# Performance work log

Measured on AMD Instinct MI355X. Metric: run time of the kernel, lower is better.

## Reference

```python
import jax, jax.numpy as jnp
import numpy as np

LN_EPS = 1e-5


def setup_inputs() -> dict:
    key = jax.random.key(0)
    k1, k2, k3, k4, k5 = jax.random.split(key, 5)
    N, E, D = 50000, 800000, 128
    feature = jax.random.normal(k1, (N, D), dtype=jnp.float32)
    snorm_n = jax.random.uniform(k2, (N, 1), dtype=jnp.float32)
    W = jax.random.normal(k3, (D, D), dtype=jnp.float32) * (1.0 / np.sqrt(D))
    ln_scale = jnp.ones((D,), dtype=jnp.float32)
    ln_bias = jnp.zeros((D,), dtype=jnp.float32)
    src = jax.random.randint(k4, (E,), 0, N, dtype=jnp.int64)
    dst = jax.random.randint(k5, (E,), 0, N, dtype=jnp.int64)
    return {"feature": feature, "snorm_n": snorm_n, "W": W,
            "ln_scale": ln_scale, "ln_bias": ln_bias, "src": src, "dst": dst}


def reference(feature, snorm_n, W, ln_scale, ln_bias, src, dst):
    N = feature.shape[0]
    # copy_src message + sum reduce: gather src features, segment-sum into dst
    msgs = feature[src]                                   # [E, D]
    h = jax.ops.segment_sum(msgs, dst, num_segments=N)    # [N, D]
    # NodeApplyModule: Linear(in_dim, out_dim, bias=False)
    h = h @ W.T                                           # [N, D]
    # graph norm
    h = h * snorm_n
    # layer norm over feature dim
    mu = jnp.mean(h, axis=-1, keepdims=True)
    var = jnp.mean(jnp.square(h - mu), axis=-1, keepdims=True)
    h = (h - mu) * jax.lax.rsqrt(var + LN_EPS) * ln_scale + ln_bias
    # activation (relu); dropout p=0 is identity in eval
    h = jax.nn.relu(h)
    return h
```

## Files before the change

kernel.cpp:

```cpp
#include <hip/hip_runtime.h>

typedef __attribute__((ext_vector_type(8))) short bf16x8;
typedef __attribute__((ext_vector_type(4))) short short4v;
typedef __attribute__((ext_vector_type(4))) float f32x4;

__device__ inline short f2bf(float x) {
    unsigned u = __builtin_bit_cast(unsigned, x);
    u += 0x7fffu + ((u >> 16) & 1u);
    return (short)(u >> 16);
}
__device__ inline float bflo(unsigned v) { return __builtin_bit_cast(float, v << 16); }
__device__ inline float bfhi(unsigned v) { return __builtin_bit_cast(float, v & 0xffff0000u); }

#define LDW  136
#define CAP  64
#define NBINS_MAX 196
#define BINSHIFT 8
#define CAPB 4864
#define RING 32
#define RSTR 33

#define POISON 0xAAAAAAAAu
__device__ inline unsigned decode_cur(unsigned raw) {
    unsigned d = raw - POISON;
    if (d < 65536u) return d;
    if (raw < 65536u) return raw;
    return 0;
}

__global__ __launch_bounds__(256) void k1_gemm_bin(
        const float* __restrict__ feat, const float* __restrict__ W,
        unsigned short* __restrict__ ft, int ntiles, int nGemm,
        const int* __restrict__ src, const int* __restrict__ dst,
        unsigned* __restrict__ binCur,
        unsigned* __restrict__ binsG,
        int E, int nbins) {
    __shared__ __align__(16) char smem[34816];
    int tid = threadIdx.x;

    if ((int)blockIdx.x < nGemm) {
        short* Wlds = (short*)smem;
        const float4* W4 = (const float4*)W;
        for (int i = tid; i < 128 * 32; i += 256) {
            int r = i >> 5, c4 = (i & 31) << 2;
            float4 w = W4[i];
            short4v s = { f2bf(w.x), f2bf(w.y), f2bf(w.z), f2bf(w.w) };
            *(short4v*)&Wlds[r * LDW + c4] = s;
        }
        __syncthreads();

        int wave = tid >> 6, lane = tid & 63;
        int l15 = lane & 15, quad = lane >> 4;

        for (int tile = blockIdx.x * 4 + wave; tile < ntiles; tile += nGemm * 4) {
            int row0 = tile << 4;
            f32x4 acc[8];
            #pragma unroll
            for (int c = 0; c < 8; ++c) acc[c] = (f32x4){0.f, 0.f, 0.f, 0.f};

            const float* arow = feat + (long long)(row0 + l15) * 128;
            #pragma unroll
            for (int t = 0; t < 4; ++t) {
                const float4* ap = (const float4*)(arow + t * 32 + quad * 8);
                float4 a0 = ap[0], a1 = ap[1];
                bf16x8 af = { f2bf(a0.x), f2bf(a0.y), f2bf(a0.z), f2bf(a0.w),
                              f2bf(a1.x), f2bf(a1.y), f2bf(a1.z), f2bf(a1.w) };
                const short* wp = &Wlds[l15 * LDW + t * 32 + quad * 8];
                #pragma unroll
                for (int c = 0; c < 8; ++c) {
                    bf16x8 bf = *(const bf16x8*)(wp + c * 16 * LDW);
                    acc[c] = __builtin_amdgcn_mfma_f32_16x16x32_bf16(af, bf, acc[c], 0, 0, 0);
                }
            }
            #pragma unroll
            for (int c = 0; c < 8; ++c) {
                int col = (c << 4) + l15;
                #pragma unroll
                for (int j = 0; j < 4; ++j)
                    ft[(long long)(row0 + quad * 4 + j) * 128 + col] =
                        (unsigned short)f2bf(acc[c][j]);
            }
        }
    } else {
        unsigned* stage = (unsigned*)smem;
        int* bcnt = (int*)(smem + NBINS_MAX * RSTR * 4);
        int* bflu = bcnt + NBINS_MAX;
        for (int i = tid; i < nbins; i += 256) { bcnt[i] = 0; bflu[i] = 0; }
        __syncthreads();

        int bid  = blockIdx.x - nGemm;
        int nB   = gridDim.x - nGemm;
        int step = nB * 256;
        int iters = (E - bid * 256 + step - 1) / step;

        int e = bid * 256 + tid;
        int d = (e < E) ? dst[e] : -1;
        int s = (e < E) ? src[e] : 0;

        for (int it = 0; it < iters; ++it) {
            int en = e + step;
            bool more = (it + 1 < iters) && (en < E);
            int dn = more ? dst[en] : -1;
            int sn = more ? src[en] : 0;

            if (d >= 0) {
                int bin = d >> BINSHIFT;
                unsigned pack = ((unsigned)(d & 255) << 16) | (unsigned)s;
                int pos = atomicAdd(&bcnt[bin], 1);
                stage[bin * RSTR + (pos & (RING - 1))] = pack;
            }
            __syncthreads();
            for (int b = tid; b < nbins; b += 256) {
                int c = bcnt[b], f = bflu[b];
                if (c - f >= 16) {
                    unsigned g = decode_cur(atomicAdd(&binCur[b], 16u));
                    if (g + 16 <= CAPB) {
                        unsigned* dp = binsG + (size_t)b * CAPB + g;
                        int s0 = f & (RING - 1);
                        #pragma unroll
                        for (int k = 0; k < 16; ++k)
                            dp[k] = stage[b * RSTR + s0 + k];
                    }
                    bflu[b] = f + 16;
                }
            }
            __syncthreads();
            e = en; d = dn; s = sn;
        }
        for (int b = tid; b < nbins; b += 256) {
            int c = bcnt[b], f = bflu[b];
            int rem = c - f;
            if (rem > 0) {
                unsigned g = decode_cur(atomicAdd(&binCur[b], (unsigned)rem));
                for (int k = 0; k < rem; ++k)
                    if (g + k < CAPB)
                        binsG[(size_t)b * CAPB + g + k] =
                            stage[b * RSTR + ((f + k) & (RING - 1))];
            }
        }
    }
}

__global__ __launch_bounds__(256) void k2_gather_ln(
        const unsigned short* __restrict__ ft,
        const unsigned* __restrict__ binCur, const unsigned* __restrict__ binsG,
        const float* __restrict__ snorm, const float* __restrict__ ln_scale,
        const float* __restrict__ ln_bias, float2* __restrict__ out,
        int N) {
    __shared__ unsigned short buck[32 * CAP];
    __shared__ int bcnt[32];
    int tid = threadIdx.x;
    int bin = blockIdx.x >> 3, oct = blockIdx.x & 7;
    int nlo = (bin << BINSHIFT) + (oct << 5);

    if (tid < 32) bcnt[tid] = 0;
    __syncthreads();

    int cnt_b = (int)decode_cur(binCur[bin]);
    if (cnt_b > CAPB) cnt_b = CAPB;
    const unsigned* bp = binsG + (size_t)bin * CAPB;
    for (int i = tid; i < cnt_b; i += 256) {
        unsigned pack = bp[i];
        int dl = pack >> 16;
        if ((dl >> 5) == oct) {
            int local = dl & 31;
            int slot = atomicAdd(&bcnt[local], 1);
            if (slot < CAP) buck[local * CAP + slot] = (unsigned short)(pack & 0xffffu);
        }
    }
    __syncthreads();

    int wave = tid >> 6, lane = tid & 63;
    const unsigned* ftp = (const unsigned*)ft;
    float2 g = ((const float2*)ln_scale)[lane];
    float2 b = ((const float2*)ln_bias)[lane];

    for (int k = 0; k < 8; ++k) {
        int local = wave * 8 + k;
        int node = nlo + local;
        if (node >= N) break;
        int deg = bcnt[local];
        if (deg > CAP) deg = CAP;
        const unsigned short* lst = &buck[local * CAP];

        float ax = 0.f, ay = 0.f;
        int i = 0;
        for (; i + 8 <= deg; i += 8) {
            ushort4 a4 = *(const ushort4*)&lst[i];
            ushort4 b4 = *(const ushort4*)&lst[i + 4];
            unsigned v0 = ftp[(int)a4.x * 64 + lane];
            unsigned v1 = ftp[(int)a4.y * 64 + lane];
            unsigned v2 = ftp[(int)a4.z * 64 + lane];
            unsigned v3 = ftp[(int)a4.w * 64 + lane];
            unsigned v4 = ftp[(int)b4.x * 64 + lane];
            unsigned v5 = ftp[(int)b4.y * 64 + lane];
            unsigned v6 = ftp[(int)b4.z * 64 + lane];
            unsigned v7 = ftp[(int)b4.w * 64 + lane];
            ax += bflo(v0) + bflo(v1) + bflo(v2) + bflo(v3)
                + bflo(v4) + bflo(v5) + bflo(v6) + bflo(v7);
            ay += bfhi(v0) + bfhi(v1) + bfhi(v2) + bfhi(v3)
                + bfhi(v4) + bfhi(v5) + bfhi(v6) + bfhi(v7);
        }
        for (; i + 4 <= deg; i += 4) {
            ushort4 s4 = *(const ushort4*)&lst[i];
            unsigned v0 = ftp[(int)s4.x * 64 + lane];
            unsigned v1 = ftp[(int)s4.y * 64 + lane];
            unsigned v2 = ftp[(int)s4.z * 64 + lane];
            unsigned v3 = ftp[(int)s4.w * 64 + lane];
            ax += bflo(v0) + bflo(v1) + bflo(v2) + bflo(v3);
            ay += bfhi(v0) + bfhi(v1) + bfhi(v2) + bfhi(v3);
        }
        for (; i < deg; ++i) {
            unsigned v = ftp[(int)lst[i] * 64 + lane];
            ax += bflo(v); ay += bfhi(v);
        }

        float sn = snorm[node];
        float vx = ax * sn, vy = ay * sn;
        float s1 = vx + vy, s2 = vx * vx + vy * vy;
        #pragma unroll
        for (int m = 1; m < 64; m <<= 1) {
            s1 += __shfl_xor(s1, m, 64);
            s2 += __shfl_xor(s2, m, 64);
        }
        float mu = s1 * (1.0f / 128.0f);
        float var = s2 * (1.0f / 128.0f) - mu * mu;
        float rs = rsqrtf(var + 1e-5f);
        float ox = fmaxf((vx - mu) * rs * g.x + b.x, 0.f);
        float oy = fmaxf((vy - mu) * rs * g.y + b.y, 0.f);
        out[(long long)node * 64 + lane] = make_float2(ox, oy);
    }
}

#define POISON_CNT_BOUND 4096u
__device__ inline int decode_cnt(unsigned raw) {
    unsigned d = raw - POISON;
    if (d < POISON_CNT_BOUND) return (int)d;
    if (raw < POISON_CNT_BOUND) return (int)raw;
    return 0;
}

__global__ __launch_bounds__(256) void fused_gemm_bucket(
        const float* __restrict__ feat, const float* __restrict__ W,
        unsigned short* __restrict__ ft, int ntiles, int nGemm,
        const int* __restrict__ src, const int* __restrict__ dst,
        int* __restrict__ cnt, unsigned short* __restrict__ esrc, int E) {
    __shared__ short Wlds[128 * LDW];
    int tid = threadIdx.x;
    if ((int)blockIdx.x < nGemm) {
        const float4* W4 = (const float4*)W;
        for (int i = tid; i < 128 * 32; i += 256) {
            int r = i >> 5, c4 = (i & 31) << 2;
            float4 w = W4[i];
            short4v s = { f2bf(w.x), f2bf(w.y), f2bf(w.z), f2bf(w.w) };
            *(short4v*)&Wlds[r * LDW + c4] = s;
        }
        __syncthreads();
        int wave = tid >> 6, lane = tid & 63;
        int l15 = lane & 15, quad = lane >> 4;
        for (int tile = blockIdx.x * 4 + wave; tile < ntiles; tile += nGemm * 4) {
            int row0 = tile << 4;
            f32x4 acc[8];
            #pragma unroll
            for (int c = 0; c < 8; ++c) acc[c] = (f32x4){0.f, 0.f, 0.f, 0.f};
            const float* arow = feat + (long long)(row0 + l15) * 128;
            #pragma unroll
            for (int t = 0; t < 4; ++t) {
                const float4* ap = (const float4*)(arow + t * 32 + quad * 8);
                float4 a0 = ap[0], a1 = ap[1];
                bf16x8 af = { f2bf(a0.x), f2bf(a0.y), f2bf(a0.z), f2bf(a0.w),
                              f2bf(a1.x), f2bf(a1.y), f2bf(a1.z), f2bf(a1.w) };
                const short* wp = &Wlds[l15 * LDW + t * 32 + quad * 8];
                #pragma unroll
                for (int c = 0; c < 8; ++c) {
                    bf16x8 bf = *(const bf16x8*)(wp + c * 16 * LDW);
                    acc[c] = __builtin_amdgcn_mfma_f32_16x16x32_bf16(af, bf, acc[c], 0, 0, 0);
                }
            }
            #pragma unroll
            for (int c = 0; c < 8; ++c) {
                int col = (c << 4) + l15;
                #pragma unroll
                for (int j = 0; j < 4; ++j)
                    ft[(long long)(row0 + quad * 4 + j) * 128 + col] =
                        (unsigned short)f2bf(acc[c][j]);
            }
        }
    } else {
        int bid = blockIdx.x - nGemm;
        int nBucket = gridDim.x - nGemm;
        for (int e = bid * 256 + tid; e < E; e += nBucket * 256) {
            int d = dst[e];
            int s = src[e];
            unsigned raw = (unsigned)atomicAdd(&cnt[d], 1);
            int slot = decode_cnt(raw);
            if (slot < CAP) esrc[d * CAP + slot] = (unsigned short)s;
        }
    }
}

__global__ __launch_bounds__(256) void gather_ln(
        const unsigned short* __restrict__ ft, const int* __restrict__ cnt,
        const unsigned short* __restrict__ esrc,
        const float* __restrict__ snorm, const float* __restrict__ ln_scale,
        const float* __restrict__ ln_bias, float2* __restrict__ out, int N) {
    int node = blockIdx.x * 4 + (threadIdx.x >> 6);
    if (node >= N) return;
    int lane = threadIdx.x & 63;
    int deg = decode_cnt((unsigned)cnt[node]);
    if (deg > CAP) deg = CAP;
    const unsigned short* lst = esrc + node * CAP;
    const unsigned* ftp = (const unsigned*)ft;
    float ax = 0.f, ay = 0.f;
    int i = 0;
    for (; i + 8 <= deg; i += 8) {
        ushort4 a4 = *(const ushort4*)&lst[i];
        ushort4 b4 = *(const ushort4*)&lst[i + 4];
        unsigned v0 = ftp[(int)a4.x * 64 + lane];
        unsigned v1 = ftp[(int)a4.y * 64 + lane];
        unsigned v2 = ftp[(int)a4.z * 64 + lane];
        unsigned v3 = ftp[(int)a4.w * 64 + lane];
        unsigned v4 = ftp[(int)b4.x * 64 + lane];
        unsigned v5 = ftp[(int)b4.y * 64 + lane];
        unsigned v6 = ftp[(int)b4.z * 64 + lane];
        unsigned v7 = ftp[(int)b4.w * 64 + lane];
        ax += bflo(v0) + bflo(v1) + bflo(v2) + bflo(v3)
            + bflo(v4) + bflo(v5) + bflo(v6) + bflo(v7);
        ay += bfhi(v0) + bfhi(v1) + bfhi(v2) + bfhi(v3)
            + bfhi(v4) + bfhi(v5) + bfhi(v6) + bfhi(v7);
    }
    for (; i + 4 <= deg; i += 4) {
        ushort4 s4 = *(const ushort4*)&lst[i];
        unsigned v0 = ftp[(int)s4.x * 64 + lane];
        unsigned v1 = ftp[(int)s4.y * 64 + lane];
        unsigned v2 = ftp[(int)s4.z * 64 + lane];
        unsigned v3 = ftp[(int)s4.w * 64 + lane];
        ax += bflo(v0) + bflo(v1) + bflo(v2) + bflo(v3);
        ay += bfhi(v0) + bfhi(v1) + bfhi(v2) + bfhi(v3);
    }
    for (; i < deg; ++i) {
        unsigned v = ftp[(int)lst[i] * 64 + lane];
        ax += bflo(v); ay += bfhi(v);
    }
    float sn = snorm[node];
    float vx = ax * sn, vy = ay * sn;
    float s1 = vx + vy, s2 = vx * vx + vy * vy;
    #pragma unroll
    for (int m = 1; m < 64; m <<= 1) {
        s1 += __shfl_xor(s1, m, 64);
        s2 += __shfl_xor(s2, m, 64);
    }
    float mu = s1 * (1.0f / 128.0f);
    float var = s2 * (1.0f / 128.0f) - mu * mu;
    float rs = rsqrtf(var + 1e-5f);
    float2 g = ((const float2*)ln_scale)[lane];
    float2 b = ((const float2*)ln_bias)[lane];
    float ox = fmaxf((vx - mu) * rs * g.x + b.x, 0.f);
    float oy = fmaxf((vy - mu) * rs * g.y + b.y, 0.f);
    out[(long long)node * 64 + lane] = make_float2(ox, oy);
}

__global__ __launch_bounds__(256) void scatter_add_kernel(
        const float4* __restrict__ feat, const int* __restrict__ src,
        const int* __restrict__ dst, float* __restrict__ h0, int E) {
    long long gid = (long long)blockIdx.x * blockDim.x + threadIdx.x;
    if (gid >= (long long)E * 32) return;
    int e = (int)(gid >> 5);
    int q = (int)(gid & 31);
    float4 f = feat[(long long)src[e] * 32 + q];
    float* p = h0 + (long long)dst[e] * 128 + (q << 2);
    atomicAdd(p + 0, f.x);
    atomicAdd(p + 1, f.y);
    atomicAdd(p + 2, f.z);
    atomicAdd(p + 3, f.w);
}

__global__ __launch_bounds__(256) void fused_gemm_ln(
        float* __restrict__ h, const float* __restrict__ W,
        const float* __restrict__ snorm, const float* __restrict__ ln_scale,
        const float* __restrict__ ln_bias, int ntiles) {
    __shared__ short Wlds[128 * LDW];
    int tid = threadIdx.x;
    const float4* W4 = (const float4*)W;
    for (int i = tid; i < 128 * 32; i += 256) {
        int r = i >> 5, c4 = (i & 31) << 2;
        float4 w = W4[i];
        short4v s = { f2bf(w.x), f2bf(w.y), f2bf(w.z), f2bf(w.w) };
        *(short4v*)&Wlds[r * LDW + c4] = s;
    }
    __syncthreads();
    int wave = tid >> 6, lane = tid & 63;
    int l15 = lane & 15, quad = lane >> 4;
    for (int tile = blockIdx.x * 4 + wave; tile < ntiles; tile += gridDim.x * 4) {
        int row0 = tile << 4;
        f32x4 acc[8];
        #pragma unroll
        for (int c = 0; c < 8; ++c) acc[c] = (f32x4){0.f, 0.f, 0.f, 0.f};
        const float* arow = h + (long long)(row0 + l15) * 128;
        #pragma unroll
        for (int t = 0; t < 4; ++t) {
            const float4* ap = (const float4*)(arow + t * 32 + quad * 8);
            float4 a0 = ap[0], a1 = ap[1];
            bf16x8 af = { f2bf(a0.x), f2bf(a0.y), f2bf(a0.z), f2bf(a0.w),
                          f2bf(a1.x), f2bf(a1.y), f2bf(a1.z), f2bf(a1.w) };
            const short* wp = &Wlds[l15 * LDW + t * 32 + quad * 8];
            #pragma unroll
            for (int c = 0; c < 8; ++c) {
                bf16x8 bf = *(const bf16x8*)(wp + c * 16 * LDW);
                acc[c] = __builtin_amdgcn_mfma_f32_16x16x32_bf16(af, bf, acc[c], 0, 0, 0);
            }
        }
        float sn[4], s1[4] = {0, 0, 0, 0}, s2[4] = {0, 0, 0, 0};
        #pragma unroll
        for (int j = 0; j < 4; ++j) sn[j] = snorm[row0 + quad * 4 + j];
        #pragma unroll
        for (int c = 0; c < 8; ++c)
            #pragma unroll
            for (int j = 0; j < 4; ++j) {
                float v = acc[c][j] * sn[j];
                acc[c][j] = v;
                s1[j] += v;
                s2[j] += v * v;
            }
        #pragma unroll
        for (int m = 1; m < 16; m <<= 1)
            #pragma unroll
            for (int j = 0; j < 4; ++j) {
                s1[j] += __shfl_xor(s1[j], m, 16);
                s2[j] += __shfl_xor(s2[j], m, 16);
            }
        float mu[4], rs[4];
        #pragma unroll
        for (int j = 0; j < 4; ++j) {
            mu[j] = s1[j] * (1.0f / 128.0f);
            float var = s2[j] * (1.0f / 128.0f) - mu[j] * mu[j];
            rs[j] = rsqrtf(var + 1e-5f);
        }
        #pragma unroll
        for (int c = 0; c < 8; ++c) {
            int col = (c << 4) + l15;
            float g = ln_scale[col], b = ln_bias[col];
            #pragma unroll
            for (int j = 0; j < 4; ++j) {
                float o = (acc[c][j] - mu[j]) * rs[j] * g + b;
                o = fmaxf(o, 0.0f);
                h[(long long)(row0 + quad * 4 + j) * 128 + col] = o;
            }
        }
    }
}

extern "C" void kernel_launch(void* const* d_in, const int* in_sizes, int n_in,
                              void* d_out, int out_size, void* d_ws, size_t ws_size,
                              hipStream_t stream) {
    const float* feature  = (const float*)d_in[0];
    const float* snorm    = (const float*)d_in[1];
    const float* W        = (const float*)d_in[2];
    const float* ln_scale = (const float*)d_in[3];
    const float* ln_bias  = (const float*)d_in[4];
    const int*   src      = (const int*)d_in[5];
    const int*   dst      = (const int*)d_in[6];
    int N = in_sizes[0] / 128;
    int E = in_sizes[5];
    float* out = (float*)d_out;
    int ntiles = N / 16;
    int nbins = (N + 255) >> 8;

    size_t need_bin = 1024 + (size_t)NBINS_MAX * CAPB * 4 + (size_t)N * 128 * 2;
    size_t need_r7  = (size_t)N * 4 + (size_t)N * CAP * 2 + (size_t)N * 128 * 2;

    bool bin_ok = ws_size >= need_bin && (N % 16) == 0 && N < 65536 &&
                  nbins <= NBINS_MAX && (size_t)nbins * 4400 >= (size_t)E;

    if (bin_ok) {
        unsigned* binCur = (unsigned*)d_ws;
        unsigned* binsG  = binCur + 256;
        unsigned short* ft = (unsigned short*)(binsG + (size_t)NBINS_MAX * CAPB);
        int nGemm = 512, nBin = 512;
        k1_gemm_bin<<<nGemm + nBin, 256, 0, stream>>>(
            feature, W, ft, ntiles, nGemm, src, dst, binCur, binsG, E, nbins);
        k2_gather_ln<<<nbins * 8, 256, 0, stream>>>(
            ft, binCur, binsG, snorm, ln_scale, ln_bias, (float2*)out, N);
    } else if (ws_size >= need_r7 && (N % 16) == 0 && N < 65536) {
        int* cnt = (int*)d_ws;
        unsigned short* esrc = (unsigned short*)(cnt + N);
        unsigned short* ft   = esrc + (size_t)N * CAP;
        fused_gemm_bucket<<<1024, 256, 0, stream>>>(
            feature, W, ft, ntiles, 320, src, dst, cnt, esrc, E);
        gather_ln<<<(N + 3) / 4, 256, 0, stream>>>(ft, cnt, esrc, snorm,
                                                   ln_scale, ln_bias, (float2*)out, N);
    } else {
        hipMemsetAsync(out, 0, (size_t)N * 128 * sizeof(float), stream);
        long long total = (long long)E * 32;
        scatter_add_kernel<<<(int)((total + 255) / 256), 256, 0, stream>>>(
            (const float4*)feature, src, dst, out, E);
        fused_gemm_ln<<<(ntiles + 3) / 4, 256, 0, stream>>>(out, W, snorm, ln_scale,
                                                            ln_bias, ntiles);
    }
}
```

Before: 144.7 us.

## Use nontemporal loads, unroll gather by 16, rebalance GEMM/bin block split

Streaming reads of the feature rows and the src/dst index arrays now use nontemporal loads, so they are less likely to push the bf16 transformed-feature table out of cache. The per-node neighbor gather loop is unrolled from 8 to 16 so more independent row loads are in flight at once. The fused kernel gives fewer blocks to the GEMM role and more to the edge-binning role. The trade-offs are higher register pressure in the gather kernel and a possibly slower GEMM role.

```diff
diff --git a/kernel.cpp b/kernel.cpp
--- a/kernel.cpp
+++ b/kernel.cpp
@@ -61,8 +61,9 @@
             const float* arow = feat + (long long)(row0 + l15) * 128;
             #pragma unroll
             for (int t = 0; t < 4; ++t) {
-                const float4* ap = (const float4*)(arow + t * 32 + quad * 8);
-                float4 a0 = ap[0], a1 = ap[1];
+                const f32x4* ap = (const f32x4*)(arow + t * 32 + quad * 8);
+                f32x4 a0 = __builtin_nontemporal_load(ap);
+                f32x4 a1 = __builtin_nontemporal_load(ap + 1);
                 bf16x8 af = { f2bf(a0.x), f2bf(a0.y), f2bf(a0.z), f2bf(a0.w),
                               f2bf(a1.x), f2bf(a1.y), f2bf(a1.z), f2bf(a1.w) };
                 const short* wp = &Wlds[l15 * LDW + t * 32 + quad * 8];
@@ -94,14 +95,14 @@
         int iters = (E - bid * 256 + step - 1) / step;
 
         int e = bid * 256 + tid;
-        int d = (e < E) ? dst[e] : -1;
-        int s = (e < E) ? src[e] : 0;
+        int d = (e < E) ? __builtin_nontemporal_load(&dst[e]) : -1;
+        int s = (e < E) ? __builtin_nontemporal_load(&src[e]) : 0;
 
         for (int it = 0; it < iters; ++it) {
             int en = e + step;
             bool more = (it + 1 < iters) && (en < E);
-            int dn = more ? dst[en] : -1;
-            int sn = more ? src[en] : 0;
+            int dn = more ? __builtin_nontemporal_load(&dst[en]) : -1;
+            int sn = more ? __builtin_nontemporal_load(&src[en]) : 0;
 
             if (d >= 0) {
                 int bin = d >> BINSHIFT;
@@ -185,21 +186,35 @@
 
         float ax = 0.f, ay = 0.f;
         int i = 0;
-        for (; i + 8 <= deg; i += 8) {
-            ushort4 a4 = *(const ushort4*)&lst[i];
-            ushort4 b4 = *(const ushort4*)&lst[i + 4];
-            unsigned v0 = ftp[(int)a4.x * 64 + lane];
-            unsigned v1 = ftp[(int)a4.y * 64 + lane];
-            unsigned v2 = ftp[(int)a4.z * 64 + lane];
-            unsigned v3 = ftp[(int)a4.w * 64 + lane];
-            unsigned v4 = ftp[(int)b4.x * 64 + lane];
-            unsigned v5 = ftp[(int)b4.y * 64 + lane];
-            unsigned v6 = ftp[(int)b4.z * 64 + lane];
-            unsigned v7 = ftp[(int)b4.w * 64 + lane];
+        for (; i + 16 <= deg; i += 16) {
+            ushort4 a0 = *(const ushort4*)&lst[i];
+            ushort4 a1 = *(const ushort4*)&lst[i + 4];
+            ushort4 a2 = *(const ushort4*)&lst[i + 8];
+            ushort4 a3 = *(const ushort4*)&lst[i + 12];
+            unsigned v0 = ftp[(int)a0.x * 64 + lane];
+            unsigned v1 = ftp[(int)a0.y * 64 + lane];
+            unsigned v2 = ftp[(int)a0.z * 64 + lane];
+            unsigned v3 = ftp[(int)a0.w * 64 + lane];
+            unsigned v4 = ftp[(int)a1.x * 64 + lane];
+            unsigned v5 = ftp[(int)a1.y * 64 + lane];
+            unsigned v6 = ftp[(int)a1.z * 64 + lane];
+            unsigned v7 = ftp[(int)a1.w * 64 + lane];
+            unsigned v8 = ftp[(int)a2.x * 64 + lane];
+            unsigned v9 = ftp[(int)a2.y * 64 + lane];
+            unsigned va = ftp[(int)a2.z * 64 + lane];
+            unsigned vb = ftp[(int)a2.w * 64 + lane];
+            unsigned vc = ftp[(int)a3.x * 64 + lane];
+            unsigned vd = ftp[(int)a3.y * 64 + lane];
+            unsigned ve = ftp[(int)a3.z * 64 + lane];
+            unsigned vf = ftp[(int)a3.w * 64 + lane];
             ax += bflo(v0) + bflo(v1) + bflo(v2) + bflo(v3)
-                + bflo(v4) + bflo(v5) + bflo(v6) + bflo(v7);
+                + bflo(v4) + bflo(v5) + bflo(v6) + bflo(v7)
+                + bflo(v8) + bflo(v9) + bflo(va) + bflo(vb)
+                + bflo(vc) + bflo(vd) + bflo(ve) + bflo(vf);
             ay += bfhi(v0) + bfhi(v1) + bfhi(v2) + bfhi(v3)
-                + bfhi(v4) + bfhi(v5) + bfhi(v6) + bfhi(v7);
+                + bfhi(v4) + bfhi(v5) + bfhi(v6) + bfhi(v7)
+                + bfhi(v8) + bfhi(v9) + bfhi(va) + bfhi(vb)
+                + bfhi(vc) + bfhi(vd) + bfhi(ve) + bfhi(vf);
         }
         for (; i + 4 <= deg; i += 4) {
             ushort4 s4 = *(const ushort4*)&lst[i];
@@ -476,7 +491,7 @@
         unsigned* binCur = (unsigned*)d_ws;
         unsigned* binsG  = binCur + 256;
         unsigned short* ft = (unsigned short*)(binsG + (size_t)NBINS_MAX * CAPB);
-        int nGemm = 512, nBin = 512;
+        int nGemm = 384, nBin = 640;
         k1_gemm_bin<<<nGemm + nBin, 256, 0, stream>>>(
             feature, W, ft, ntiles, nGemm, src, dst, binCur, binsG, E, nbins);
         k2_gather_ln<<<nbins * 8, 256, 0, stream>>>(
@@ -490,7 +505,7 @@
         gather_ln<<<(N + 3) / 4, 256, 0, stream>>>(ft, cnt, esrc, snorm,
                                                    ln_scale, ln_bias, (float2*)out, N);
     } else {
-        hipMemsetAsync(out, 0, (size_t)N * 128 * sizeof(float), stream);
+        (void)hipMemsetAsync(out, 0, (size_t)N * 128 * sizeof(float), stream);
         long long total = (long long)E * 32;
         scatter_add_kernel<<<(int)((total + 255) / 256), 256, 0, stream>>>(
             (const float4*)feature, src, dst, out, E);
```

After: 147.2 us. Within noise of the previous version (+1.7%).
